# Kernel tuning notes

Hardware: AMD Instinct MI355X
Metric: run time of the kernel (lower is better)

## Reference

```python
import jax, jax.numpy as jnp
import numpy as np

FM = 80            # feature_maps
N_ROUNDS = 32
NORM_EPS = 1e-3
LOSS_EPS = 1e-8


def _relu6(x):
    return jnp.clip(x, 0.0, 6.0)


def _norm(x):
    # tf.nn.moments over axis 0 + batch_normalization (no scale/offset)
    mean = jnp.mean(x, axis=0, keepdims=True)
    var = jnp.var(x, axis=0, keepdims=True)
    return (x - mean) * jax.lax.rsqrt(var + NORM_EPS)


def setup_inputs() -> dict:
    key = jax.random.key(0)
    n_vars, n_clauses, n_graphs, lits_per_clause = 100000, 420000, 100, 3
    n_cells = n_clauses * lits_per_clause
    ks = jax.random.split(key, 24)

    lit_var = jax.random.randint(ks[0], (n_cells,), 0, n_vars, dtype=jnp.int32)
    lit_neg = jax.random.randint(ks[1], (n_cells,), 0, 2, dtype=jnp.int32)
    clause_idx = jnp.repeat(jnp.arange(n_clauses, dtype=jnp.int32), lits_per_clause)
    clause_graph = jnp.repeat(jnp.arange(n_graphs, dtype=jnp.int32), n_clauses // n_graphs)

    def dense(k, fi, fo):
        return jax.random.normal(k, (fi, fo), jnp.float32) / np.sqrt(fi)

    inp = dict(
        lit_var=lit_var, lit_neg=lit_neg, clause_idx=clause_idx, clause_graph=clause_graph,
        n_vars=n_vars, n_clauses=n_clauses, n_graphs=n_graphs,
        L_init_scale=jnp.float32(1.0 / np.sqrt(FM)),
        C_init_scale=jnp.float32(1.0 / np.sqrt(FM)),
        LC_scale=jnp.float32(0.1), CL_scale=jnp.float32(0.1),
        # L_update MLP: in=3*FM (L, CL_msgs, flip(L)) -> hidden 3*FM relu6 -> FM
        Lu_W0=dense(ks[2], 3 * FM, 3 * FM), Lu_b0=jnp.zeros((3 * FM,), jnp.float32),
        Lu_W1=dense(ks[3], 3 * FM, FM),     Lu_b1=jnp.zeros((FM,), jnp.float32),
        # C_update MLP: in=2*FM (C, LC_msgs) -> hidden 2*FM relu6 -> FM
        Cu_W0=dense(ks[4], 2 * FM, 2 * FM), Cu_b0=jnp.zeros((2 * FM,), jnp.float32),
        Cu_W1=dense(ks[5], 2 * FM, FM),     Cu_b1=jnp.zeros((FM,), jnp.float32),
        # V_score MLP: in=2*FM -> 3 hidden relu6 layers of 2*FM -> 1
        Vs_W0=dense(ks[6], 2 * FM, 2 * FM), Vs_b0=jnp.zeros((2 * FM,), jnp.float32),
        Vs_W1=dense(ks[7], 2 * FM, 2 * FM), Vs_b1=jnp.zeros((2 * FM,), jnp.float32),
        Vs_W2=dense(ks[8], 2 * FM, 2 * FM), Vs_b2=jnp.zeros((2 * FM,), jnp.float32),
        Vs_W3=dense(ks[9], 2 * FM, 1),      Vs_b3=jnp.zeros((1,), jnp.float32),
    )
    return inp


def reference(lit_var, lit_neg, clause_idx, clause_graph, n_vars, n_clauses, n_graphs,
              L_init_scale, C_init_scale, LC_scale, CL_scale,
              Lu_W0, Lu_b0, Lu_W1, Lu_b1,
              Cu_W0, Cu_b0, Cu_W1, Cu_b1,
              Vs_W0, Vs_b0, Vs_W1, Vs_b1, Vs_W2, Vs_b2, Vs_W3, Vs_b3):
    n_lits = 2 * n_vars
    lit_row = lit_var + lit_neg * n_vars          # row in L for each cell
    sign = (1 - 2 * lit_neg).astype(jnp.float32)  # +1 positive literal, -1 negated

    def mlp_L(x):
        return _relu6(x @ Lu_W0 + Lu_b0) @ Lu_W1 + Lu_b1

    def mlp_C(x):
        return _relu6(x @ Cu_W0 + Cu_b0) @ Cu_W1 + Cu_b1

    def v_score(x):
        h = _relu6(x @ Vs_W0 + Vs_b0)
        h = _relu6(h @ Vs_W1 + Vs_b1)
        h = _relu6(h @ Vs_W2 + Vs_b2)
        return h @ Vs_W3 + Vs_b3

    def flip(L):
        return jnp.concatenate([L[n_vars:], L[:n_vars]], axis=0)

    def per_round_loss(logits):
        # softplus_mixed_loss over ragged clauses of signed literals
        lit_vals = logits[lit_var, 0] * sign                         # [n_cells]
        clause_sum = jax.ops.segment_sum(jax.nn.softplus(lit_vals), clause_idx,
                                         num_segments=n_clauses)     # [n_clauses]
        vc = jnp.exp(-clause_sum)
        per_clause = vc * (-jnp.log(1.0 - vc + LOSS_EPS))
        per_graph = jax.ops.segment_sum(per_clause, clause_graph, num_segments=n_graphs)
        return jnp.sum(jnp.sqrt(per_graph + 1e-6))

    L0 = jnp.ones((n_lits, FM), jnp.float32) * L_init_scale
    C0 = jnp.ones((n_clauses, FM), jnp.float32) * C_init_scale

    def round_fn(carry, _):
        L, C, loss = carry
        # CL^T @ L  (sparse gather + segment-sum over clause cells)
        LC_msgs = jax.ops.segment_sum(L[lit_row], clause_idx, num_segments=n_clauses) * LC_scale
        C = _norm(mlp_C(jnp.concatenate([C, LC_msgs], axis=-1)))
        # adj @ C  (scatter-add clause features back to literal rows)
        CL_msgs = jax.ops.segment_sum(C[clause_idx], lit_row, num_segments=n_lits) * CL_scale
        L = _norm(mlp_L(jnp.concatenate([L, CL_msgs, flip(L)], axis=-1)))
        V = jnp.concatenate([L[:n_vars], L[n_vars:]], axis=1)        # [n_vars, 2*FM]
        logits = v_score(V)
        loss = loss + per_round_loss(logits)
        return (L, C, loss), None

    (L, C, loss), _ = jax.lax.scan(round_fn, (L0, C0, jnp.float32(0.0)), None, length=N_ROUNDS)
    # final-round logits (recomputed from the final L state, identical math)
    logits = v_score(jnp.concatenate([L[:n_vars], L[n_vars:]], axis=1))
    return logits, loss / N_ROUNDS
```

## Files before the change

kernel.cpp:

```cpp
#include <hip/hip_runtime.h>
#include <math.h>


#define NROUNDS 32
#define NORM_EPS 1e-3f
#define LOSS_EPS 1e-8f

static constexpr int NV_CONST = 100000;
static constexpr int NG_CONST = 100;

typedef __attribute__((ext_vector_type(8))) short short8;
typedef __attribute__((ext_vector_type(4))) float f32x4;

__device__ __forceinline__ short f2bf(float f) {
    union { float f; unsigned u; } x; x.f = f;
    unsigned r = x.u + 0x7fffu + ((x.u >> 16) & 1u);
    return (short)(r >> 16);
}
__device__ __forceinline__ float bf2f(short s) {
    union { unsigned u; float f; } x; x.u = ((unsigned)(unsigned short)s) << 16;
    return x.f;
}


__global__ void k_zero_i(int* __restrict__ p, int n) {
    int i = blockIdx.x * 256 + threadIdx.x;
    if (i < n) p[i] = 0;
}
__global__ void k_fill_b(short* __restrict__ p, int n, const float* __restrict__ vp) {
    int i = blockIdx.x * 256 + threadIdx.x;
    if (i < n) p[i] = f2bf(*vp);
}
__global__ void k_copy_int(int* __restrict__ dst, const int* __restrict__ src, int n) {
    int i = blockIdx.x * 256 + threadIdx.x;
    if (i < n) dst[i] = src[i];
}
__global__ void k_init_slabs(float* __restrict__ slabC, float* __restrict__ slabL,
                             float* __restrict__ loss_a, float nclf) {
    int i = blockIdx.x * 256 + threadIdx.x;
    if (i < 33 * 160) {
        slabC[i] = (i >= 80 && i < 160) ? nclf * (1.f - NORM_EPS) : 0.f;
        slabL[i] = 0.f;
    }
    if (i == 0) loss_a[0] = 0.f;
}

__global__ void k_litrow(const int* __restrict__ lit_var, const int* __restrict__ lit_neg,
                         int* __restrict__ litrow, int* __restrict__ counts,
                         int ncell, int nv) {
    int i = blockIdx.x * 256 + threadIdx.x;
    if (i < ncell) {
        int r = lit_var[i] + lit_neg[i] * nv;
        litrow[i] = r;
        atomicAdd(&counts[r], 1);
    }
}

__launch_bounds__(1024)
__global__ void k_scan4(const int* __restrict__ counts, int* __restrict__ row_ptr,
                        int n, int total) {
    __shared__ int sd[1024];
    __shared__ int carry;
    int tid = threadIdx.x;
    if (tid == 0) carry = 0;
    __syncthreads();
    for (int base = 0; base < n; base += 4096) {
        int i0 = base + tid * 4;
        int a0 = (i0 + 0 < n) ? counts[i0 + 0] : 0;
        int a1 = (i0 + 1 < n) ? counts[i0 + 1] : 0;
        int a2 = (i0 + 2 < n) ? counts[i0 + 2] : 0;
        int a3 = (i0 + 3 < n) ? counts[i0 + 3] : 0;
        int s = a0 + a1 + a2 + a3;
        sd[tid] = s;
        __syncthreads();
        for (int off = 1; off < 1024; off <<= 1) {
            int t = (tid >= off) ? sd[tid - off] : 0;
            __syncthreads();
            sd[tid] += t;
            __syncthreads();
        }
        int excl = carry + sd[tid] - s;
        if (i0 + 0 < n) row_ptr[i0 + 0] = excl;
        if (i0 + 1 < n) row_ptr[i0 + 1] = excl + a0;
        if (i0 + 2 < n) row_ptr[i0 + 2] = excl + a0 + a1;
        if (i0 + 3 < n) row_ptr[i0 + 3] = excl + a0 + a1 + a2;
        __syncthreads();
        if (tid == 0) carry += sd[1023];
        __syncthreads();
    }
    if (tid == 0) row_ptr[n] = total;
}

__global__ void k_fill_csr(const int* __restrict__ litrow, const int* __restrict__ clause_idx,
                           int* __restrict__ cursor, int* __restrict__ cl_of, int ncell) {
    int i = blockIdx.x * 256 + threadIdx.x;
    if (i < ncell) {
        int r = litrow[i];
        int pos = atomicAdd(&cursor[r], 1);
        cl_of[pos] = clause_idx[i];
    }
}

__global__ void k_pack_w(const float* __restrict__ W, short* __restrict__ Wp,
                         int K, int N, int KB, int NB) {
    int t = blockIdx.x * 256 + threadIdx.x;
    int tot = NB * KB * 64;
    if (t >= tot) return;
    int lane = t & 63;
    int kb = (t >> 6) % KB;
    int nb = t / (64 * KB);
    int quad = lane >> 4, l15 = lane & 15;
    int n = nb * 16 + l15;
#pragma unroll
    for (int j = 0; j < 8; ++j) {
        int k = kb * 32 + quad * 8 + j;
        float f = (k < K && n < N) ? W[(size_t)k * N + n] : 0.f;
        Wp[(size_t)t * 8 + j] = f2bf(f);
    }
}


template <int KB, int NB>
__device__ __forceinline__ void mfma_layer(const short* lds, int SK,
                                           const short8* __restrict__ Wp,
                                           f32x4* acc, int lane, int arow) {
    const int quad8 = (lane >> 4) * 8;
    short8 a[KB];
#pragma unroll
    for (int kb = 0; kb < KB; ++kb)
        a[kb] = *(const short8*)(lds + arow * SK + kb * 32 + quad8);
#pragma unroll
    for (int kb = 0; kb < KB; ++kb)
#pragma unroll
        for (int nb = 0; nb < NB; ++nb)
            acc[nb] = __builtin_amdgcn_mfma_f32_16x16x32_bf16(
                a[kb], Wp[(nb * KB + kb) * 64 + lane], acc[nb], 0, 0, 0);
}

template <int NB>
__device__ __forceinline__ void write_hidden(short* ldsH, int SKH, const f32x4* acc,
                                             const float* __restrict__ bias,
                                             int l15, int quad, int wr0) {
#pragma unroll
    for (int nb = 0; nb < NB; ++nb) {
        int c = nb * 16 + l15;
        float bv = bias[c];
#pragma unroll
        for (int reg = 0; reg < 4; ++reg) {
            int row = wr0 + quad * 4 + reg;
            float v = acc[nb][reg] + bv;
            v = fminf(fmaxf(v, 0.f), 6.f);
            ldsH[row * SKH + c] = f2bf(v);
        }
    }
}

__device__ __forceinline__ void load_stats(const float* __restrict__ slab, float Minv,
                                           float* sS, int tid) {
    if (tid < 80) {
        float m = slab[tid] * Minv;
        float v = slab[80 + tid] * Minv - m * m;
        sS[tid] = m;
        sS[80 + tid] = rsqrtf(v + NORM_EPS);
    }
}

__launch_bounds__(256, 2)
__global__ void k_c_update(short* __restrict__ Cb, const short* __restrict__ Lb,
                           const int* __restrict__ litrow, const float* __restrict__ scp,
                           const short8* __restrict__ W0p, const float* __restrict__ b0,
                           const short8* __restrict__ W1p, const float* __restrict__ b1,
                           const float* __restrict__ prevSlab, float* __restrict__ nextSlab,
                           float Minv, int ncl, int nv) {
    constexpr int SK = 168;
    __shared__ short lds[64 * SK];
    __shared__ float sred[160], sC[160];
    const int lane = threadIdx.x, wy = threadIdx.y, tid = wy * 64 + lane;
    const int r0 = blockIdx.x * 64;
    const int rows = (ncl - r0 < 64) ? (ncl - r0) : 64;

    if (tid < 160) sred[tid] = 0.f;
    load_stats(prevSlab, Minv, sC, tid);
    __syncthreads();

    const float s = *scp;
    const short8* Cb8 = (const short8*)Cb;
    const short8* Lb8 = (const short8*)Lb;
    for (int it = tid; it < 64 * 20; it += 256) {
        int lr = it / 20, c = it % 20;
        int cl = r0 + ((lr < rows) ? lr : rows - 1);
        if (c < 10) {
            short8 v = Cb8[(size_t)cl * 10 + c];
            int col = c * 8;
            short8 o;
#pragma unroll
            for (int j = 0; j < 8; ++j)
                o[j] = f2bf((bf2f(v[j]) - sC[col + j]) * sC[80 + col + j]);
            *(short8*)(lds + lr * SK + col) = o;
        } else {
            int cc = c - 10, b = cl * 3;
            int ra = litrow[b], rb = litrow[b + 1], rc = litrow[b + 2];
            short8 va = Lb8[(ra < nv) ? (size_t)ra * 20 + cc : (size_t)(ra - nv) * 20 + 10 + cc];
            short8 vb = Lb8[(rb < nv) ? (size_t)rb * 20 + cc : (size_t)(rb - nv) * 20 + 10 + cc];
            short8 vc = Lb8[(rc < nv) ? (size_t)rc * 20 + cc : (size_t)(rc - nv) * 20 + 10 + cc];
            short8 o;
#pragma unroll
            for (int j = 0; j < 8; ++j)
                o[j] = f2bf((bf2f(va[j]) + bf2f(vb[j]) + bf2f(vc[j])) * s);
            *(short8*)(lds + lr * SK + 80 + cc * 8) = o;
        }
    }
    __syncthreads();

    const int quad = lane >> 4, l15 = lane & 15, wr0 = wy * 16, arow = wr0 + l15;

    f32x4 acc[10];
#pragma unroll
    for (int nb = 0; nb < 10; ++nb) { f32x4 z = {0.f, 0.f, 0.f, 0.f}; acc[nb] = z; }
    mfma_layer<5, 10>(lds, SK, W0p, acc, lane, arow);
    write_hidden<10>(lds, SK, acc, b0, l15, quad, wr0);

    f32x4 acc2[5];
#pragma unroll
    for (int nb = 0; nb < 5; ++nb) { f32x4 z = {0.f, 0.f, 0.f, 0.f}; acc2[nb] = z; }
    mfma_layer<5, 5>(lds, SK, W1p, acc2, lane, arow);

#pragma unroll
    for (int nb = 0; nb < 5; ++nb) {
        int cc = nb * 16 + l15;
        float bv = b1[cc];
        float s1 = 0.f, s2 = 0.f;
#pragma unroll
        for (int reg = 0; reg < 4; ++reg) {
            int lr = wr0 + quad * 4 + reg;
            if (lr < rows) {
                float v = acc2[nb][reg] + bv;
                Cb[(size_t)(r0 + lr) * 80 + cc] = f2bf(v);
                s1 += v; s2 += v * v;
            }
        }
        s1 += __shfl_xor(s1, 16); s1 += __shfl_xor(s1, 32);
        s2 += __shfl_xor(s2, 16); s2 += __shfl_xor(s2, 32);
        if (quad == 0) { atomicAdd(&sred[cc], s1); atomicAdd(&sred[80 + cc], s2); }
    }
    __syncthreads();
    if (tid < 160) atomicAdd(&nextSlab[tid], sred[tid]);
}

__global__ void k_cl_gather(const short* __restrict__ Cb, const int* __restrict__ row_ptr,
                            const int* __restrict__ cl_of, const float* __restrict__ scp,
                            const float* __restrict__ slab, float Minv,
                            short* __restrict__ CLb, int nl) {
    __shared__ float sC[160];
    load_stats(slab, Minv, sC, threadIdx.x);
    __syncthreads();
    int idx = blockIdx.x * 256 + threadIdx.x;
    if (idx >= nl * 20) return;
    int r = idx / 20, q = idx % 20;
    int p0 = row_ptr[r], p1 = row_ptr[r + 1];
    float a0 = 0.f, a1 = 0.f, a2 = 0.f, a3 = 0.f;
    const short4* Cb4 = (const short4*)Cb;
    int p = p0;
    for (; p + 2 <= p1; p += 2) {
        short4 v0 = Cb4[(size_t)cl_of[p] * 20 + q];
        short4 v1 = Cb4[(size_t)cl_of[p + 1] * 20 + q];
        a0 += bf2f(v0.x) + bf2f(v1.x);
        a1 += bf2f(v0.y) + bf2f(v1.y);
        a2 += bf2f(v0.z) + bf2f(v1.z);
        a3 += bf2f(v0.w) + bf2f(v1.w);
    }
    if (p < p1) {
        short4 v0 = Cb4[(size_t)cl_of[p] * 20 + q];
        a0 += bf2f(v0.x); a1 += bf2f(v0.y); a2 += bf2f(v0.z); a3 += bf2f(v0.w);
    }
    float n = (float)(p1 - p0), s = *scp;
    int col = 4 * q;
    short4 o;
    o.x = f2bf((a0 - n * sC[col])     * sC[80 + col]     * s);
    o.y = f2bf((a1 - n * sC[col + 1]) * sC[80 + col + 1] * s);
    o.z = f2bf((a2 - n * sC[col + 2]) * sC[80 + col + 2] * s);
    o.w = f2bf((a3 - n * sC[col + 3]) * sC[80 + col + 3] * s);
    ((short4*)CLb)[idx] = o;
}

__launch_bounds__(256, 2)
__global__ void k_l_update(short* __restrict__ Lraw, const short* __restrict__ Lb,
                           const short* __restrict__ CLb,
                           const short8* __restrict__ W0p, const float* __restrict__ b0,
                           const short8* __restrict__ W1p, const float* __restrict__ b1,
                           float* __restrict__ nextSlab, int nv) {
    constexpr int SK = 264;
    __shared__ short lds[64 * SK];
    __shared__ float sred[160];
    const int lane = threadIdx.x, wy = threadIdx.y, tid = wy * 64 + lane;
    const int vb = blockIdx.x * 32;

    if (tid < 160) sred[tid] = 0.f;
    __syncthreads();

    const short8* Lb8  = (const short8*)Lb;
    const short8* CLb8 = (const short8*)CLb;
    for (int it = tid; it < 64 * 32; it += 256) {
        int lr = it >> 5, c = it & 31;
        short* dst = lds + lr * SK;
        int v = (lr < 32) ? vb + lr : vb + (lr - 32);
        int half0 = (lr < 32) ? 0 : 10;
        if (c < 10) {
            *(short8*)(dst + c * 8) = Lb8[(size_t)v * 20 + half0 + c];
        } else if (c < 20) {
            int r = (lr < 32) ? vb + lr : vb + nv + (lr - 32);
            *(short8*)(dst + 80 + (c - 10) * 8) = CLb8[(size_t)r * 10 + (c - 10)];
        } else if (c < 30) {
            *(short8*)(dst + 160 + (c - 20) * 8) = Lb8[(size_t)v * 20 + (10 - half0) + (c - 20)];
        } else {
            short8 z = {0, 0, 0, 0, 0, 0, 0, 0};
            *(short8*)(dst + 240 + (c - 30) * 8) = z;
        }
    }
    __syncthreads();

    const int quad = lane >> 4, l15 = lane & 15, wr0 = wy * 16, arow = wr0 + l15;

    f32x4 acc[15];
#pragma unroll
    for (int nb = 0; nb < 15; ++nb) { f32x4 z = {0.f, 0.f, 0.f, 0.f}; acc[nb] = z; }
    mfma_layer<8, 15>(lds, SK, W0p, acc, lane, arow);
    write_hidden<15>(lds, SK, acc, b0, l15, quad, wr0);
    {
        int row = wr0 + (lane >> 2);
        int c = 240 + (lane & 3) * 4;
        short4 z; z.x = 0; z.y = 0; z.z = 0; z.w = 0;
        *(short4*)(lds + row * SK + c) = z;
    }

    f32x4 acc2[5];
#pragma unroll
    for (int nb = 0; nb < 5; ++nb) { f32x4 z = {0.f, 0.f, 0.f, 0.f}; acc2[nb] = z; }
    mfma_layer<8, 5>(lds, SK, W1p, acc2, lane, arow);

#pragma unroll
    for (int nb = 0; nb < 5; ++nb) {
        int cc = nb * 16 + l15;
        float bv = b1[cc];
        float s1 = 0.f, s2 = 0.f;
#pragma unroll
        for (int reg = 0; reg < 4; ++reg) {
            int lr = wr0 + quad * 4 + reg;
            int rabs = (lr < 32) ? vb + lr : vb + nv + (lr - 32);
            float v = acc2[nb][reg] + bv;
            Lraw[(size_t)rabs * 80 + cc] = f2bf(v);
            s1 += v; s2 += v * v;
        }
        s1 += __shfl_xor(s1, 16); s1 += __shfl_xor(s1, 32);
        s2 += __shfl_xor(s2, 16); s2 += __shfl_xor(s2, 32);
        if (quad == 0) { atomicAdd(&sred[cc], s1); atomicAdd(&sred[80 + cc], s2); }
    }
    __syncthreads();
    if (tid < 160) atomicAdd(&nextSlab[tid], sred[tid]);
}

__launch_bounds__(256, 2)
__global__ void k_v_head(const short* __restrict__ Lraw, const float* __restrict__ slab,
                         float Minv,
                         const short8* __restrict__ W0p, const float* __restrict__ b0,
                         const short8* __restrict__ W1p, const float* __restrict__ b1,
                         const short8* __restrict__ W2p, const float* __restrict__ b2,
                         const float* __restrict__ W3, const float* __restrict__ b3,
                         float* __restrict__ logits, short* __restrict__ Lb, int nv) {
    constexpr int SK = 168;
    __shared__ short lds[64 * SK];
    __shared__ float sW3[160], sL[160];
    const int lane = threadIdx.x, wy = threadIdx.y, tid = wy * 64 + lane;
    const int v0 = blockIdx.x * 64;
    const int cnt = (nv - v0 < 64) ? (nv - v0) : 64;

    if (tid < 160) sW3[tid] = W3[tid];
    load_stats(slab, Minv, sL, tid);
    __syncthreads();

    const short8* Lraw8 = (const short8*)Lraw;
    for (int it = tid; it < 64 * 20; it += 256) {
        int lr = it / 20, c = it % 20;
        int v = v0 + ((lr < cnt) ? lr : cnt - 1);
        int row = (c < 10) ? v : v + nv;
        int cc = (c < 10) ? c : c - 10;
        int col = cc * 8;
        short8 x = Lraw8[(size_t)row * 10 + cc];
        short8 o;
#pragma unroll
        for (int j = 0; j < 8; ++j)
            o[j] = f2bf((bf2f(x[j]) - sL[col + j]) * sL[80 + col + j]);
        *(short8*)(lds + lr * SK + c * 8) = o;
        if (lr < cnt) *(short8*)(Lb + (size_t)v * 160 + c * 8) = o;
    }
    __syncthreads();

    const int quad = lane >> 4, l15 = lane & 15, wr0 = wy * 16, arow = wr0 + l15;

    f32x4 acc[10];
#pragma unroll
    for (int nb = 0; nb < 10; ++nb) { f32x4 z = {0.f, 0.f, 0.f, 0.f}; acc[nb] = z; }
    mfma_layer<5, 10>(lds, SK, W0p, acc, lane, arow);
    write_hidden<10>(lds, SK, acc, b0, l15, quad, wr0);

#pragma unroll
    for (int nb = 0; nb < 10; ++nb) { f32x4 z = {0.f, 0.f, 0.f, 0.f}; acc[nb] = z; }
    mfma_layer<5, 10>(lds, SK, W1p, acc, lane, arow);
    write_hidden<10>(lds, SK, acc, b1, l15, quad, wr0);

#pragma unroll
    for (int nb = 0; nb < 10; ++nb) { f32x4 z = {0.f, 0.f, 0.f, 0.f}; acc[nb] = z; }
    mfma_layer<5, 10>(lds, SK, W2p, acc, lane, arow);
    write_hidden<10>(lds, SK, acc, b2, l15, quad, wr0);
    __syncthreads();

    int lrow = tid >> 2, t4 = tid & 3;
    float v = 0.f;
    for (int c = t4; c < 160; c += 4) v += bf2f(lds[lrow * SK + c]) * sW3[c];
    v += __shfl_down(v, 2, 4);
    v += __shfl_down(v, 1, 4);
    if (t4 == 0 && lrow < cnt) logits[v0 + lrow] = v + b3[0];
}

__device__ __forceinline__ float softplusf(float x) {
    return fmaxf(x, 0.f) + log1pf(expf(-fabsf(x)));
}

__global__ void k_loss(const float* __restrict__ logits, const int* __restrict__ lit_var,
                       const int* __restrict__ lit_neg, float* __restrict__ loss_acc,
                       int cpg) {
    const int g = blockIdx.x;
    const int tid = threadIdx.x;
    float part = 0.f;
    int cend = (g + 1) * cpg;
    for (int c = g * cpg + tid; c < cend; c += 256) {
        float cs = 0.f;
#pragma unroll
        for (int t = 0; t < 3; ++t) {
            int i = c * 3 + t;
            float sign = lit_neg[i] ? -1.f : 1.f;
            cs += softplusf(logits[lit_var[i]] * sign);
        }
        float vc = expf(-cs);
        part += vc * (-log1pf(LOSS_EPS - vc));
    }
    __shared__ float red[256];
    red[tid] = part;
    __syncthreads();
    for (int s = 128; s > 0; s >>= 1) {
        if (tid < s) red[tid] += red[tid + s];
        __syncthreads();
    }
    if (tid == 0) atomicAdd(loss_acc, sqrtf(red[0] + 1e-6f));
}

__global__ void k_output(float* __restrict__ dout, const float* __restrict__ logits,
                         const float* __restrict__ loss_acc, int nv) {
    int i = blockIdx.x * 256 + threadIdx.x;
    if (i < nv) dout[i] = logits[i];
    else if (i == nv) dout[i] = loss_acc[0] * (1.f / (float)NROUNDS);
}


extern "C" void kernel_launch(void* const* d_in, const int* in_sizes, int n_in,
                              void* d_out, int out_size, void* d_ws, size_t ws_size,
                              hipStream_t stream) {
    const int* lit_var    = (const int*)d_in[0];
    const int* lit_neg    = (const int*)d_in[1];
    const int* clause_idx = (const int*)d_in[2];
    const float* Lscale = (const float*)d_in[7];
    const float* Cscale = (const float*)d_in[8];
    const float* LCs    = (const float*)d_in[9];
    const float* CLs    = (const float*)d_in[10];
    const float* LuW0 = (const float*)d_in[11]; const float* Lub0 = (const float*)d_in[12];
    const float* LuW1 = (const float*)d_in[13]; const float* Lub1 = (const float*)d_in[14];
    const float* CuW0 = (const float*)d_in[15]; const float* Cub0 = (const float*)d_in[16];
    const float* CuW1 = (const float*)d_in[17]; const float* Cub1 = (const float*)d_in[18];
    const float* VsW0 = (const float*)d_in[19]; const float* Vsb0 = (const float*)d_in[20];
    const float* VsW1 = (const float*)d_in[21]; const float* Vsb1 = (const float*)d_in[22];
    const float* VsW2 = (const float*)d_in[23]; const float* Vsb2 = (const float*)d_in[24];
    const float* VsW3 = (const float*)d_in[25]; const float* Vsb3 = (const float*)d_in[26];

    const int ncell = in_sizes[0];
    const int ncl   = in_sizes[3];
    const int nv    = NV_CONST;
    const int nl    = 2 * nv;
    const int ng    = NG_CONST;

    size_t off = 0;
    auto A = [&](size_t bytes) -> void* {
        void* q = (char*)d_ws + off;
        off = (off + bytes + 255) & ~(size_t)255;
        return q;
    };
    short* Cb    = (short*)A((size_t)ncl * 80 * 2);
    short* Lraw  = (short*)A((size_t)nl * 80 * 2);
    short* Lb    = (short*)A((size_t)nv * 160 * 2);
    short* CLb   = (short*)A((size_t)nl * 80 * 2);
    float* logits = (float*)A((size_t)nv * 4);
    float* slabC  = (float*)A(33 * 160 * 4);
    float* slabL  = (float*)A(33 * 160 * 4);
    float* loss_a = (float*)A(256);
    int* litrow  = (int*)A((size_t)ncell * 4);
    int* row_ptr = (int*)A((size_t)(nl + 1) * 4);
    int* tmp     = (int*)A((size_t)nl * 4);
    int* cl_of   = (int*)A((size_t)ncell * 4);
    short* CuW0p = (short*)A((size_t)10 * 5 * 64 * 16);
    short* CuW1p = (short*)A((size_t)5  * 5 * 64 * 16);
    short* LuW0p = (short*)A((size_t)15 * 8 * 64 * 16);
    short* LuW1p = (short*)A((size_t)5  * 8 * 64 * 16);
    short* VsW0p = (short*)A((size_t)10 * 5 * 64 * 16);
    short* VsW1p = (short*)A((size_t)10 * 5 * 64 * 16);
    short* VsW2p = (short*)A((size_t)10 * 5 * 64 * 16);

    const dim3 B64x4(64, 4, 1);

    k_zero_i<<<(nl + 255) / 256, 256, 0, stream>>>(tmp, nl);
    k_init_slabs<<<(33 * 160 + 255) / 256, 256, 0, stream>>>(slabC, slabL, loss_a, (float)ncl);
    k_litrow<<<(ncell + 255) / 256, 256, 0, stream>>>(lit_var, lit_neg, litrow, tmp, ncell, nv);
    k_scan4<<<1, 1024, 0, stream>>>(tmp, row_ptr, nl, ncell);
    k_copy_int<<<(nl + 255) / 256, 256, 0, stream>>>(tmp, row_ptr, nl);
    k_fill_csr<<<(ncell + 255) / 256, 256, 0, stream>>>(litrow, clause_idx, tmp, cl_of, ncell);
    k_fill_b<<<(ncl * 80 + 255) / 256, 256, 0, stream>>>(Cb, ncl * 80, Cscale);
    k_fill_b<<<(nl * 80 + 255) / 256, 256, 0, stream>>>(Lraw, nl * 80, Lscale);
    k_fill_b<<<(nv * 160 + 255) / 256, 256, 0, stream>>>(Lb, nv * 160, Lscale);
    k_pack_w<<<(10 * 5 * 64 + 255) / 256, 256, 0, stream>>>(CuW0, CuW0p, 160, 160, 5, 10);
    k_pack_w<<<(5  * 5 * 64 + 255) / 256, 256, 0, stream>>>(CuW1, CuW1p, 160, 80, 5, 5);
    k_pack_w<<<(15 * 8 * 64 + 255) / 256, 256, 0, stream>>>(LuW0, LuW0p, 240, 240, 8, 15);
    k_pack_w<<<(5  * 8 * 64 + 255) / 256, 256, 0, stream>>>(LuW1, LuW1p, 240, 80, 8, 5);
    k_pack_w<<<(10 * 5 * 64 + 255) / 256, 256, 0, stream>>>(VsW0, VsW0p, 160, 160, 5, 10);
    k_pack_w<<<(10 * 5 * 64 + 255) / 256, 256, 0, stream>>>(VsW1, VsW1p, 160, 160, 5, 10);
    k_pack_w<<<(10 * 5 * 64 + 255) / 256, 256, 0, stream>>>(VsW2, VsW2p, 160, 160, 5, 10);

    const int cblk = (ncl + 63) / 64;
    const int lblk = nv / 32;
    const int vblk = (nv + 63) / 64;
    const int gblk = (nl * 20 + 255) / 256;
    const float MinvC = 1.f / (float)ncl;
    const float MinvL = 1.f / (float)nl;

    for (int r = 0; r < NROUNDS; ++r) {
        float* sCr  = slabC + (size_t)r * 160;
        float* sCr1 = slabC + (size_t)(r + 1) * 160;
        float* sLr1 = slabL + (size_t)(r + 1) * 160;
        k_c_update<<<cblk, B64x4, 0, stream>>>(
            Cb, Lb, litrow, LCs, (const short8*)CuW0p, Cub0, (const short8*)CuW1p, Cub1,
            sCr, sCr1, MinvC, ncl, nv);
        k_cl_gather<<<gblk, 256, 0, stream>>>(Cb, row_ptr, cl_of, CLs, sCr1, MinvC, CLb, nl);
        k_l_update<<<lblk, B64x4, 0, stream>>>(
            Lraw, Lb, CLb, (const short8*)LuW0p, Lub0, (const short8*)LuW1p, Lub1, sLr1, nv);
        k_v_head<<<vblk, B64x4, 0, stream>>>(
            Lraw, sLr1, MinvL, (const short8*)VsW0p, Vsb0, (const short8*)VsW1p, Vsb1,
            (const short8*)VsW2p, Vsb2, VsW3, Vsb3, logits, Lb, nv);
        k_loss<<<ng, 256, 0, stream>>>(logits, lit_var, lit_neg, loss_a, ncl / ng);
    }

    k_output<<<(nv + 1 + 255) / 256, 256, 0, stream>>>((float*)d_out, logits, loss_a, nv);
}
```

Baseline: 16.33 ms.

## Split clause gather into separate kernel, widen CL gather, batch tile loads

Moves the literal-to-clause gather out of the MLP kernel into a standalone high-occupancy kernel that writes an LC buffer, using precomputed per-cell row offsets. The CL gather is widened from short4 to short8 with a 4-way unrolled accumulation. The tile-staging loops in the C, L and V kernels now issue all global loads before writing LDS, so more loads are in flight. The cost is an extra kernel launch per round and an extra LC buffer round trip through memory.

```diff
diff --git a/kernel.cpp b/kernel.cpp
--- a/kernel.cpp
+++ b/kernel.cpp
@@ -46,12 +46,13 @@
 }
 
 __global__ void k_litrow(const int* __restrict__ lit_var, const int* __restrict__ lit_neg,
-                         int* __restrict__ litrow, int* __restrict__ counts,
-                         int ncell, int nv) {
+                         int* __restrict__ litrow, int* __restrict__ lofs,
+                         int* __restrict__ counts, int ncell, int nv) {
     int i = blockIdx.x * 256 + threadIdx.x;
     if (i < ncell) {
         int r = lit_var[i] + lit_neg[i] * nv;
         litrow[i] = r;
+        lofs[i] = (r < nv) ? r * 20 : (r - nv) * 20 + 10;
         atomicAdd(&counts[r], 1);
     }
 }
@@ -165,13 +166,33 @@
     }
 }
 
+__launch_bounds__(256)
+__global__ void k_lc_gather(const short* __restrict__ Lb, const int* __restrict__ lofs,
+                            const float* __restrict__ scp, short* __restrict__ LCb,
+                            int ncl) {
+    int idx = blockIdx.x * 256 + threadIdx.x;
+    if (idx >= ncl * 10) return;
+    int cl = idx / 10, c8 = idx - cl * 10;
+    int b = cl * 3;
+    int oa = lofs[b], ob = lofs[b + 1], oc = lofs[b + 2];
+    const short8* Lb8 = (const short8*)Lb;
+    short8 va = Lb8[(size_t)oa + c8];
+    short8 vb = Lb8[(size_t)ob + c8];
+    short8 vc = Lb8[(size_t)oc + c8];
+    float s = *scp;
+    short8 o;
+#pragma unroll
+    for (int j = 0; j < 8; ++j)
+        o[j] = f2bf((bf2f(va[j]) + bf2f(vb[j]) + bf2f(vc[j])) * s);
+    ((short8*)LCb)[idx] = o;
+}
+
 __launch_bounds__(256, 2)
-__global__ void k_c_update(short* __restrict__ Cb, const short* __restrict__ Lb,
-                           const int* __restrict__ litrow, const float* __restrict__ scp,
+__global__ void k_c_update(short* __restrict__ Cb, const short* __restrict__ LCb,
                            const short8* __restrict__ W0p, const float* __restrict__ b0,
                            const short8* __restrict__ W1p, const float* __restrict__ b1,
                            const float* __restrict__ prevSlab, float* __restrict__ nextSlab,
-                           float Minv, int ncl, int nv) {
+                           float Minv, int ncl) {
     constexpr int SK = 168;
     __shared__ short lds[64 * SK];
     __shared__ float sred[160], sC[160];
@@ -183,31 +204,29 @@
     load_stats(prevSlab, Minv, sC, tid);
     __syncthreads();
 
-    const float s = *scp;
-    const short8* Cb8 = (const short8*)Cb;
-    const short8* Lb8 = (const short8*)Lb;
-    for (int it = tid; it < 64 * 20; it += 256) {
-        int lr = it / 20, c = it % 20;
+    const short8* Cb8  = (const short8*)Cb;
+    const short8* LCb8 = (const short8*)LCb;
+    short8 vals[5];
+#pragma unroll
+    for (int u = 0; u < 5; ++u) {
+        int it = tid + u * 256;
+        int lr = it / 20, c = it - lr * 20;
         int cl = r0 + ((lr < rows) ? lr : rows - 1);
+        vals[u] = (c < 10) ? Cb8[(size_t)cl * 10 + c] : LCb8[(size_t)cl * 10 + (c - 10)];
+    }
+#pragma unroll
+    for (int u = 0; u < 5; ++u) {
+        int it = tid + u * 256;
+        int lr = it / 20, c = it - lr * 20;
         if (c < 10) {
-            short8 v = Cb8[(size_t)cl * 10 + c];
             int col = c * 8;
             short8 o;
 #pragma unroll
             for (int j = 0; j < 8; ++j)
-                o[j] = f2bf((bf2f(v[j]) - sC[col + j]) * sC[80 + col + j]);
+                o[j] = f2bf((bf2f(vals[u][j]) - sC[col + j]) * sC[80 + col + j]);
             *(short8*)(lds + lr * SK + col) = o;
         } else {
-            int cc = c - 10, b = cl * 3;
-            int ra = litrow[b], rb = litrow[b + 1], rc = litrow[b + 2];
-            short8 va = Lb8[(ra < nv) ? (size_t)ra * 20 + cc : (size_t)(ra - nv) * 20 + 10 + cc];
-            short8 vb = Lb8[(rb < nv) ? (size_t)rb * 20 + cc : (size_t)(rb - nv) * 20 + 10 + cc];
-            short8 vc = Lb8[(rc < nv) ? (size_t)rc * 20 + cc : (size_t)(rc - nv) * 20 + 10 + cc];
-            short8 o;
-#pragma unroll
-            for (int j = 0; j < 8; ++j)
-                o[j] = f2bf((bf2f(va[j]) + bf2f(vb[j]) + bf2f(vc[j])) * s);
-            *(short8*)(lds + lr * SK + 80 + cc * 8) = o;
+            *(short8*)(lds + lr * SK + 80 + (c - 10) * 8) = vals[u];
         }
     }
     __syncthreads();
@@ -247,6 +266,7 @@
     if (tid < 160) atomicAdd(&nextSlab[tid], sred[tid]);
 }
 
+__launch_bounds__(256)
 __global__ void k_cl_gather(const short* __restrict__ Cb, const int* __restrict__ row_ptr,
                             const int* __restrict__ cl_of, const float* __restrict__ scp,
                             const float* __restrict__ slab, float Minv,
@@ -255,32 +275,36 @@
     load_stats(slab, Minv, sC, threadIdx.x);
     __syncthreads();
     int idx = blockIdx.x * 256 + threadIdx.x;
-    if (idx >= nl * 20) return;
-    int r = idx / 20, q = idx % 20;
+    if (idx >= nl * 10) return;
+    int r = idx / 10, c8 = idx - r * 10;
     int p0 = row_ptr[r], p1 = row_ptr[r + 1];
-    float a0 = 0.f, a1 = 0.f, a2 = 0.f, a3 = 0.f;
-    const short4* Cb4 = (const short4*)Cb;
+    float a[8];
+#pragma unroll
+    for (int j = 0; j < 8; ++j) a[j] = 0.f;
+    const short8* Cb8 = (const short8*)Cb;
     int p = p0;
-    for (; p + 2 <= p1; p += 2) {
-        short4 v0 = Cb4[(size_t)cl_of[p] * 20 + q];
-        short4 v1 = Cb4[(size_t)cl_of[p + 1] * 20 + q];
-        a0 += bf2f(v0.x) + bf2f(v1.x);
-        a1 += bf2f(v0.y) + bf2f(v1.y);
-        a2 += bf2f(v0.z) + bf2f(v1.z);
-        a3 += bf2f(v0.w) + bf2f(v1.w);
-    }
-    if (p < p1) {
-        short4 v0 = Cb4[(size_t)cl_of[p] * 20 + q];
-        a0 += bf2f(v0.x); a1 += bf2f(v0.y); a2 += bf2f(v0.z); a3 += bf2f(v0.w);
+    for (; p + 4 <= p1; p += 4) {
+        int i0 = cl_of[p], i1 = cl_of[p + 1], i2 = cl_of[p + 2], i3 = cl_of[p + 3];
+        short8 v0 = Cb8[(size_t)i0 * 10 + c8];
+        short8 v1 = Cb8[(size_t)i1 * 10 + c8];
+        short8 v2 = Cb8[(size_t)i2 * 10 + c8];
+        short8 v3 = Cb8[(size_t)i3 * 10 + c8];
+#pragma unroll
+        for (int j = 0; j < 8; ++j)
+            a[j] += (bf2f(v0[j]) + bf2f(v1[j])) + (bf2f(v2[j]) + bf2f(v3[j]));
+    }
+    for (; p < p1; ++p) {
+        short8 v = Cb8[(size_t)cl_of[p] * 10 + c8];
+#pragma unroll
+        for (int j = 0; j < 8; ++j) a[j] += bf2f(v[j]);
     }
     float n = (float)(p1 - p0), s = *scp;
-    int col = 4 * q;
-    short4 o;
-    o.x = f2bf((a0 - n * sC[col])     * sC[80 + col]     * s);
-    o.y = f2bf((a1 - n * sC[col + 1]) * sC[80 + col + 1] * s);
-    o.z = f2bf((a2 - n * sC[col + 2]) * sC[80 + col + 2] * s);
-    o.w = f2bf((a3 - n * sC[col + 3]) * sC[80 + col + 3] * s);
-    ((short4*)CLb)[idx] = o;
+    int col = c8 * 8;
+    short8 o;
+#pragma unroll
+    for (int j = 0; j < 8; ++j)
+        o[j] = f2bf((a[j] - n * sC[col + j]) * sC[80 + col + j] * s);
+    ((short8*)CLb)[idx] = o;
 }
 
 __launch_bounds__(256, 2)
@@ -300,22 +324,32 @@
 
     const short8* Lb8  = (const short8*)Lb;
     const short8* CLb8 = (const short8*)CLb;
-    for (int it = tid; it < 64 * 32; it += 256) {
+    short8 vals[8];
+#pragma unroll
+    for (int u = 0; u < 8; ++u) {
+        int it = tid + u * 256;
         int lr = it >> 5, c = it & 31;
-        short* dst = lds + lr * SK;
         int v = (lr < 32) ? vb + lr : vb + (lr - 32);
         int half0 = (lr < 32) ? 0 : 10;
         if (c < 10) {
-            *(short8*)(dst + c * 8) = Lb8[(size_t)v * 20 + half0 + c];
+            vals[u] = Lb8[(size_t)v * 20 + half0 + c];
         } else if (c < 20) {
             int r = (lr < 32) ? vb + lr : vb + nv + (lr - 32);
-            *(short8*)(dst + 80 + (c - 10) * 8) = CLb8[(size_t)r * 10 + (c - 10)];
+            vals[u] = CLb8[(size_t)r * 10 + (c - 10)];
         } else if (c < 30) {
-            *(short8*)(dst + 160 + (c - 20) * 8) = Lb8[(size_t)v * 20 + (10 - half0) + (c - 20)];
+            vals[u] = Lb8[(size_t)v * 20 + (10 - half0) + (c - 20)];
         } else {
             short8 z = {0, 0, 0, 0, 0, 0, 0, 0};
-            *(short8*)(dst + 240 + (c - 30) * 8) = z;
+            vals[u] = z;
         }
+    }
+#pragma unroll
+    for (int u = 0; u < 8; ++u) {
+        int it = tid + u * 256;
+        int lr = it >> 5, c = it & 31;
+        int o = (c < 10) ? c * 8 : (c < 20) ? 80 + (c - 10) * 8
+              : (c < 30) ? 160 + (c - 20) * 8 : 240 + (c - 30) * 8;
+        *(short8*)(lds + lr * SK + o) = vals[u];
     }
     __syncthreads();
 
@@ -379,17 +413,27 @@
     __syncthreads();
 
     const short8* Lraw8 = (const short8*)Lraw;
-    for (int it = tid; it < 64 * 20; it += 256) {
-        int lr = it / 20, c = it % 20;
+    short8 vals[5];
+#pragma unroll
+    for (int u = 0; u < 5; ++u) {
+        int it = tid + u * 256;
+        int lr = it / 20, c = it - lr * 20;
         int v = v0 + ((lr < cnt) ? lr : cnt - 1);
         int row = (c < 10) ? v : v + nv;
         int cc = (c < 10) ? c : c - 10;
+        vals[u] = Lraw8[(size_t)row * 10 + cc];
+    }
+#pragma unroll
+    for (int u = 0; u < 5; ++u) {
+        int it = tid + u * 256;
+        int lr = it / 20, c = it - lr * 20;
+        int v = v0 + ((lr < cnt) ? lr : cnt - 1);
+        int cc = (c < 10) ? c : c - 10;
         int col = cc * 8;
-        short8 x = Lraw8[(size_t)row * 10 + cc];
         short8 o;
 #pragma unroll
         for (int j = 0; j < 8; ++j)
-            o[j] = f2bf((bf2f(x[j]) - sL[col + j]) * sL[80 + col + j]);
+            o[j] = f2bf((bf2f(vals[u][j]) - sL[col + j]) * sL[80 + col + j]);
         *(short8*)(lds + lr * SK + c * 8) = o;
         if (lr < cnt) *(short8*)(Lb + (size_t)v * 160 + c * 8) = o;
     }
@@ -497,11 +541,13 @@
     short* Lraw  = (short*)A((size_t)nl * 80 * 2);
     short* Lb    = (short*)A((size_t)nv * 160 * 2);
     short* CLb   = (short*)A((size_t)nl * 80 * 2);
+    short* LCb   = (short*)A((size_t)ncl * 80 * 2);
     float* logits = (float*)A((size_t)nv * 4);
     float* slabC  = (float*)A(33 * 160 * 4);
     float* slabL  = (float*)A(33 * 160 * 4);
     float* loss_a = (float*)A(256);
     int* litrow  = (int*)A((size_t)ncell * 4);
+    int* lofs    = (int*)A((size_t)ncell * 4);
     int* row_ptr = (int*)A((size_t)(nl + 1) * 4);
     int* tmp     = (int*)A((size_t)nl * 4);
     int* cl_of   = (int*)A((size_t)ncell * 4);
@@ -517,7 +563,7 @@
 
     k_zero_i<<<(nl + 255) / 256, 256, 0, stream>>>(tmp, nl);
     k_init_slabs<<<(33 * 160 + 255) / 256, 256, 0, stream>>>(slabC, slabL, loss_a, (float)ncl);
-    k_litrow<<<(ncell + 255) / 256, 256, 0, stream>>>(lit_var, lit_neg, litrow, tmp, ncell, nv);
+    k_litrow<<<(ncell + 255) / 256, 256, 0, stream>>>(lit_var, lit_neg, litrow, lofs, tmp, ncell, nv);
     k_scan4<<<1, 1024, 0, stream>>>(tmp, row_ptr, nl, ncell);
     k_copy_int<<<(nl + 255) / 256, 256, 0, stream>>>(tmp, row_ptr, nl);
     k_fill_csr<<<(ncell + 255) / 256, 256, 0, stream>>>(litrow, clause_idx, tmp, cl_of, ncell);
@@ -532,10 +578,11 @@
     k_pack_w<<<(10 * 5 * 64 + 255) / 256, 256, 0, stream>>>(VsW1, VsW1p, 160, 160, 5, 10);
     k_pack_w<<<(10 * 5 * 64 + 255) / 256, 256, 0, stream>>>(VsW2, VsW2p, 160, 160, 5, 10);
 
-    const int cblk = (ncl + 63) / 64;
-    const int lblk = nv / 32;
-    const int vblk = (nv + 63) / 64;
-    const int gblk = (nl * 20 + 255) / 256;
+    const int cblk  = (ncl + 63) / 64;
+    const int lblk  = nv / 32;
+    const int vblk  = (nv + 63) / 64;
+    const int lcblk = (ncl * 10 + 255) / 256;
+    const int clblk = (nl * 10 + 255) / 256;
     const float MinvC = 1.f / (float)ncl;
     const float MinvL = 1.f / (float)nl;
 
@@ -543,10 +590,11 @@
         float* sCr  = slabC + (size_t)r * 160;
         float* sCr1 = slabC + (size_t)(r + 1) * 160;
         float* sLr1 = slabL + (size_t)(r + 1) * 160;
+        k_lc_gather<<<lcblk, 256, 0, stream>>>(Lb, lofs, LCs, LCb, ncl);
         k_c_update<<<cblk, B64x4, 0, stream>>>(
-            Cb, Lb, litrow, LCs, (const short8*)CuW0p, Cub0, (const short8*)CuW1p, Cub1,
-            sCr, sCr1, MinvC, ncl, nv);
-        k_cl_gather<<<gblk, 256, 0, stream>>>(Cb, row_ptr, cl_of, CLs, sCr1, MinvC, CLb, nl);
+            Cb, LCb, (const short8*)CuW0p, Cub0, (const short8*)CuW1p, Cub1,
+            sCr, sCr1, MinvC, ncl);
+        k_cl_gather<<<clblk, 256, 0, stream>>>(Cb, row_ptr, cl_of, CLs, sCr1, MinvC, CLb, nl);
         k_l_update<<<lblk, B64x4, 0, stream>>>(
             Lraw, Lb, CLb, (const short8*)LuW0p, Lub0, (const short8*)LuW1p, Lub1, sLr1, nv);
         k_v_head<<<vblk, B64x4, 0, stream>>>(
```

Result: slower. 17.18 ms (+5.2%).
